# Performance work log

Measured on AMD Instinct MI355X. Metric: run time of the kernel, lower is better.

Reference implementation:

```python
import jax, jax.numpy as jnp
import numpy as np

N, E, G = 50000, 800000, 64
D, DE, DIN, L = 64, 4, 11, 2


def _lin(x, w, b):
    return x @ w + b


def _bn(x, g, b, eps=1e-5):
    # BatchNorm1d in training mode: biased batch statistics over dim 0
    m = x.mean(0)
    v = x.var(0)
    return (x - m) * jax.lax.rsqrt(v + eps) * g + b


def setup_inputs() -> dict:
    key = jax.random.key(0)
    ks = iter(jax.random.split(key, 64))

    def rn(shape, s=0.05):
        return jax.random.normal(next(ks), shape, jnp.float32) * s

    inp = dict(
        x=rn((N, DIN), 1.0),
        pos=rn((N, 3), 1.0),
        edge_attr=rn((E, DE), 1.0),
        edge_index=jax.random.randint(next(ks), (2, E), 0, N),
        batch=jnp.sort(jax.random.randint(next(ks), (N,), 0, G)),
        lin_in_w=rn((DIN, D)), lin_in_b=jnp.zeros((D,), jnp.float32),
        lin_pred_w=rn((D, 1)), lin_pred_b=jnp.zeros((1,), jnp.float32),
        # per-layer stacked params (leading dim L)
        msg_w1=rn((L, 2 * D + DE + 1, D)), msg_b1=jnp.zeros((L, D), jnp.float32),
        msg_g1=jnp.ones((L, D), jnp.float32), msg_be1=jnp.zeros((L, D), jnp.float32),
        msg_w2=rn((L, D, D)), msg_b2=jnp.zeros((L, D), jnp.float32),
        msg_g2=jnp.ones((L, D), jnp.float32), msg_be2=jnp.zeros((L, D), jnp.float32),
        pos_w1=rn((L, D, D)), pos_b1=jnp.zeros((L, D), jnp.float32),
        pos_g=jnp.ones((L, D), jnp.float32), pos_be=jnp.zeros((L, D), jnp.float32),
        pos_w2=rn((L, D, 1)), pos_b2=jnp.zeros((L, 1), jnp.float32),
        upd_w1=rn((L, 2 * D, D)), upd_b1=jnp.zeros((L, D), jnp.float32),
        upd_g1=jnp.ones((L, D), jnp.float32), upd_be1=jnp.zeros((L, D), jnp.float32),
        upd_w2=rn((L, D, D)), upd_b2=jnp.zeros((L, D), jnp.float32),
        upd_g2=jnp.ones((L, D), jnp.float32), upd_be2=jnp.zeros((L, D), jnp.float32),
    )
    return inp


def reference(x, pos, edge_attr, edge_index, batch,
              lin_in_w, lin_in_b, lin_pred_w, lin_pred_b,
              msg_w1, msg_b1, msg_g1, msg_be1, msg_w2, msg_b2, msg_g2, msg_be2,
              pos_w1, pos_b1, pos_g, pos_be, pos_w2, pos_b2,
              upd_w1, upd_b1, upd_g1, upd_be1, upd_w2, upd_b2, upd_g2, upd_be2):
    src, dst = edge_index[0], edge_index[1]  # h_j = h[src], h_i = h[dst]
    h = x @ lin_in_w + lin_in_b
    p = pos
    deg = jnp.maximum(jax.ops.segment_sum(jnp.ones((E,), h.dtype), dst, N), 1.0)
    for l in range(L):
        h_i, h_j = h[dst], h[src]          # (E, D) gathers
        pd = p[dst] - p[src]               # (E, 3)
        radial = jnp.sum(pd * pd, axis=1, keepdims=True)  # (E, 1)
        m = jnp.concatenate([h_i, h_j, radial, edge_attr], -1)  # (E, 2D+DE+1)
        m = jax.nn.relu(_bn(_lin(m, msg_w1[l], msg_b1[l]), msg_g1[l], msg_be1[l]))
        m = jax.nn.relu(_bn(_lin(m, msg_w2[l], msg_b2[l]), msg_g2[l], msg_be2[l]))
        s = jax.nn.relu(_bn(_lin(m, pos_w1[l], pos_b1[l]), pos_g[l], pos_be[l]))
        s = _lin(s, pos_w2[l], pos_b2[l])  # (E, 1) scalar gate
        pos_upd = pd * s                   # (E, 3)
        m_aggr = jax.ops.segment_sum(m, dst, N)                    # sum aggr
        p_aggr = jax.ops.segment_sum(pos_upd, dst, N) / deg[:, None]  # mean aggr
        u = jnp.concatenate([h, m_aggr], -1)
        u = jax.nn.relu(_bn(_lin(u, upd_w1[l], upd_b1[l]), upd_g1[l], upd_be1[l]))
        u = jax.nn.relu(_bn(_lin(u, upd_w2[l], upd_b2[l]), upd_g2[l], upd_be2[l]))
        h = h + u          # residual on node features (MPNNModel style)
        p = p + p_aggr     # position update from layer
    cnt = jnp.maximum(jax.ops.segment_sum(jnp.ones((N,), h.dtype), batch, G), 1.0)
    h_graph = jax.ops.segment_sum(h, batch, G) / cnt[:, None]  # global_mean_pool
    out = h_graph @ lin_pred_w + lin_pred_b
    return out.reshape(-1)
```

## Files before the change

### kernel.cpp

```cpp
#include <hip/hip_runtime.h>

#define Nn 50000
#define Ee 800000
#define Gg 64
#define Dd 64
#define KIN 133
#define ES 68
#define EPS 1e-5f

typedef unsigned short u16;

__device__ __forceinline__ u16 f2bf(float f) {
    union { float f; unsigned u; } v; v.f = f;
    unsigned r = (v.u + 0x7FFFu + ((v.u >> 16) & 1u)) >> 16;
    return (u16)r;
}
__device__ __forceinline__ float bf2f(u16 s) {
    union { unsigned u; float f; } v; v.u = ((unsigned)s) << 16;
    return v.f;
}


__global__ __launch_bounds__(256) void k_lin_in(const float* __restrict__ x,
    const float* __restrict__ W, const float* __restrict__ B, float* __restrict__ h)
{
    __shared__ float Ws[11 * 64];
    __shared__ float Bs[64];
    int t = threadIdx.x;
    for (int i = t; i < 11 * 64; i += 256) Ws[i] = W[i];
    if (t < 64) Bs[t] = B[t];
    __syncthreads();
    int i = blockIdx.x * 256 + t;
    if (i < Nn * 64) {
        int n = i >> 6, c = i & 63;
        float acc = Bs[c];
        #pragma unroll
        for (int k = 0; k < 11; k++) acc += x[n * 11 + k] * Ws[k * 64 + c];
        h[i] = acc;
    }
}

__global__ __launch_bounds__(256) void k_deg(const int* __restrict__ ei, float* __restrict__ deg)
{
    int e = blockIdx.x * 256 + threadIdx.x;
    if (e < Ee) atomicAdd(&deg[ei[Ee + e]], 1.f);
}

__global__ __launch_bounds__(256) void k_cnt(const int* __restrict__ batch, float* __restrict__ cnt)
{
    int n = blockIdx.x * 256 + threadIdx.x;
    if (n < Nn) atomicAdd(&cnt[batch[n]], 1.f);
}


__global__ __launch_bounds__(256) void k_edge_lin1(
    const float* __restrict__ h, const float* __restrict__ p,
    const float* __restrict__ ea, const int* __restrict__ ei,
    const float* __restrict__ W, const float* __restrict__ B,
    u16* __restrict__ ybuf, float* __restrict__ stats_out)
{
    __shared__ float Ws[KIN * 64];
    __shared__ float Bs[64];
    __shared__ float in_t[KIN * ES];
    int t = threadIdx.x;
    for (int i = t; i < KIN * 64; i += 256) Ws[i] = W[i];
    if (t < 64) Bs[t] = B[t];
    int tx = t & 15, ty = t >> 4;
    int c = t & 63, eg = t >> 6;
    float ssum[4] = {0, 0, 0, 0}, ssq[4] = {0, 0, 0, 0};
    for (int tile = blockIdx.x; tile < Ee / 64; tile += gridDim.x) {
        int te = tile * 64;
        __syncthreads();
        for (int e = eg; e < 64; e += 4) {
            int sr = ei[te + e], ds = ei[Ee + te + e];
            in_t[c * ES + e]        = h[(size_t)ds * 64 + c];
            in_t[(64 + c) * ES + e] = h[(size_t)sr * 64 + c];
        }
        if (t < 64) {
            int e = t;
            int sr = ei[te + e], ds = ei[Ee + te + e];
            float dx = p[ds * 3 + 0] - p[sr * 3 + 0];
            float dy = p[ds * 3 + 1] - p[sr * 3 + 1];
            float dz = p[ds * 3 + 2] - p[sr * 3 + 2];
            in_t[128 * ES + e] = dx * dx + dy * dy + dz * dz;
            float4 a4 = *(const float4*)&ea[(size_t)(te + e) * 4];
            in_t[129 * ES + e] = a4.x;
            in_t[130 * ES + e] = a4.y;
            in_t[131 * ES + e] = a4.z;
            in_t[132 * ES + e] = a4.w;
        }
        __syncthreads();
        float acc[4][4];
        #pragma unroll
        for (int i = 0; i < 4; i++)
            #pragma unroll
            for (int j = 0; j < 4; j++) acc[i][j] = Bs[4 * ty + j];
        for (int k = 0; k < KIN; k++) {
            float av[4], wv[4];
            *(float4*)av = *(const float4*)&in_t[k * ES + 4 * tx];
            *(float4*)wv = *(const float4*)&Ws[k * 64 + 4 * ty];
            #pragma unroll
            for (int i = 0; i < 4; i++)
                #pragma unroll
                for (int j = 0; j < 4; j++)
                    acc[i][j] += av[i] * wv[j];
        }
        #pragma unroll
        for (int i = 0; i < 4; i++) {
            size_t e = (size_t)te + 4 * tx + i;
            ushort4 o;
            o.x = f2bf(acc[i][0]); o.y = f2bf(acc[i][1]);
            o.z = f2bf(acc[i][2]); o.w = f2bf(acc[i][3]);
            *(ushort4*)&ybuf[e * 64 + 4 * ty] = o;
            float r0 = bf2f(o.x), r1 = bf2f(o.y), r2 = bf2f(o.z), r3 = bf2f(o.w);
            ssum[0] += r0; ssum[1] += r1; ssum[2] += r2; ssum[3] += r3;
            ssq[0] += r0 * r0; ssq[1] += r1 * r1; ssq[2] += r2 * r2; ssq[3] += r3 * r3;
        }
    }
    #pragma unroll
    for (int j = 0; j < 4; j++) {
        float s = ssum[j], q = ssq[j];
        #pragma unroll
        for (int o2 = 1; o2 < 16; o2 <<= 1) { s += __shfl_xor(s, o2); q += __shfl_xor(q, o2); }
        if (tx == 0) {
            atomicAdd(&stats_out[4 * ty + j], s);
            atomicAdd(&stats_out[64 + 4 * ty + j], q);
        }
    }
}


template<int AGGR>
__global__ __launch_bounds__(256) void k_edge_lin64(
    const float* __restrict__ stats_in, const float* __restrict__ gg,
    const float* __restrict__ be,
    const float* __restrict__ W, const float* __restrict__ B,
    const int* __restrict__ ei, float* __restrict__ magg,
    u16* __restrict__ ybuf, float* __restrict__ stats_out)
{
    __shared__ float Ws[64 * 64];
    __shared__ float As[64], Cs[64], Bs[64];
    __shared__ float in_t[64 * ES];
    int t = threadIdx.x;
    if (t < 64) {
        float mean = stats_in[t] * (1.f / Ee);
        float var  = stats_in[64 + t] * (1.f / Ee) - mean * mean;
        float a = gg[t] * rsqrtf(var + EPS);
        As[t] = a; Cs[t] = be[t] - mean * a; Bs[t] = B[t];
    }
    for (int i = t; i < 64 * 64; i += 256) Ws[i] = W[i];
    int tx = t & 15, ty = t >> 4;
    int c = t & 63, eg = t >> 6;
    float ssum[4] = {0, 0, 0, 0}, ssq[4] = {0, 0, 0, 0};
    for (int tile = blockIdx.x; tile < Ee / 64; tile += gridDim.x) {
        int te = tile * 64;
        __syncthreads();
        for (int e = eg; e < 64; e += 4) {
            float y = bf2f(ybuf[(size_t)(te + e) * 64 + c]);
            in_t[c * ES + e] = fmaxf(As[c] * y + Cs[c], 0.f);
        }
        __syncthreads();
        float acc[4][4];
        #pragma unroll
        for (int i = 0; i < 4; i++)
            #pragma unroll
            for (int j = 0; j < 4; j++) acc[i][j] = Bs[4 * ty + j];
        for (int k = 0; k < 64; k++) {
            float av[4], wv[4];
            *(float4*)av = *(const float4*)&in_t[k * ES + 4 * tx];
            *(float4*)wv = *(const float4*)&Ws[k * 64 + 4 * ty];
            #pragma unroll
            for (int i = 0; i < 4; i++)
                #pragma unroll
                for (int j = 0; j < 4; j++)
                    acc[i][j] += av[i] * wv[j];
        }
        if (AGGR) {
            for (int e = eg; e < 64; e += 4) {
                int ds = ei[Ee + te + e];
                atomicAdd(&magg[(size_t)ds * 64 + c], in_t[c * ES + e]);
            }
        }
        #pragma unroll
        for (int i = 0; i < 4; i++) {
            size_t e = (size_t)te + 4 * tx + i;
            ushort4 o;
            o.x = f2bf(acc[i][0]); o.y = f2bf(acc[i][1]);
            o.z = f2bf(acc[i][2]); o.w = f2bf(acc[i][3]);
            *(ushort4*)&ybuf[e * 64 + 4 * ty] = o;
            float r0 = bf2f(o.x), r1 = bf2f(o.y), r2 = bf2f(o.z), r3 = bf2f(o.w);
            ssum[0] += r0; ssum[1] += r1; ssum[2] += r2; ssum[3] += r3;
            ssq[0] += r0 * r0; ssq[1] += r1 * r1; ssq[2] += r2 * r2; ssq[3] += r3 * r3;
        }
    }
    #pragma unroll
    for (int j = 0; j < 4; j++) {
        float s = ssum[j], q = ssq[j];
        #pragma unroll
        for (int o2 = 1; o2 < 16; o2 <<= 1) { s += __shfl_xor(s, o2); q += __shfl_xor(q, o2); }
        if (tx == 0) {
            atomicAdd(&stats_out[4 * ty + j], s);
            atomicAdd(&stats_out[64 + 4 * ty + j], q);
        }
    }
}


__global__ __launch_bounds__(256) void k_pos2(
    const float* __restrict__ stats_in, const float* __restrict__ gg, const float* __restrict__ be,
    const float* __restrict__ W2, const float* __restrict__ B2,
    const float* __restrict__ p, const int* __restrict__ ei,
    const u16* __restrict__ ybuf, float* __restrict__ pagg)
{
    __shared__ float As[64], Cs[64], Ws[64];
    int t = threadIdx.x;
    if (t < 64) {
        float mean = stats_in[t] * (1.f / Ee);
        float var  = stats_in[64 + t] * (1.f / Ee) - mean * mean;
        float a = gg[t] * rsqrtf(var + EPS);
        As[t] = a; Cs[t] = be[t] - mean * a; Ws[t] = W2[t];
    }
    __syncthreads();
    int e = blockIdx.x * 256 + t;
    if (e >= Ee) return;
    float acc = B2[0];
    const u16* row = &ybuf[(size_t)e * 64];
    #pragma unroll
    for (int u = 0; u < 16; u++) {
        ushort4 y4 = *(const ushort4*)&row[4 * u];
        acc += fmaxf(As[4 * u + 0] * bf2f(y4.x) + Cs[4 * u + 0], 0.f) * Ws[4 * u + 0]
             + fmaxf(As[4 * u + 1] * bf2f(y4.y) + Cs[4 * u + 1], 0.f) * Ws[4 * u + 1]
             + fmaxf(As[4 * u + 2] * bf2f(y4.z) + Cs[4 * u + 2], 0.f) * Ws[4 * u + 2]
             + fmaxf(As[4 * u + 3] * bf2f(y4.w) + Cs[4 * u + 3], 0.f) * Ws[4 * u + 3];
    }
    int sr = ei[e], ds = ei[Ee + e];
    float dx = p[ds * 3 + 0] - p[sr * 3 + 0];
    float dy = p[ds * 3 + 1] - p[sr * 3 + 1];
    float dz = p[ds * 3 + 2] - p[sr * 3 + 2];
    atomicAdd(&pagg[ds * 3 + 0], dx * acc);
    atomicAdd(&pagg[ds * 3 + 1], dy * acc);
    atomicAdd(&pagg[ds * 3 + 2], dz * acc);
}


__global__ __launch_bounds__(256) void k_node_lin1(
    const float* __restrict__ h, const float* __restrict__ magg,
    const float* __restrict__ W, const float* __restrict__ B,
    float* __restrict__ yn, float* __restrict__ stats_out)
{
    __shared__ float Ws[128 * 64];
    __shared__ float Bs[64];
    __shared__ float in_t[128 * ES];
    int t = threadIdx.x;
    for (int i = t; i < 128 * 64; i += 256) Ws[i] = W[i];
    if (t < 64) Bs[t] = B[t];
    int tx = t & 15, ty = t >> 4, c = t & 63, eg = t >> 6;
    float ssum[4] = {0, 0, 0, 0}, ssq[4] = {0, 0, 0, 0};
    int nT = (Nn + 63) / 64;
    for (int tile = blockIdx.x; tile < nT; tile += gridDim.x) {
        int te = tile * 64;
        __syncthreads();
        for (int e = eg; e < 64; e += 4) {
            int n = te + e;
            bool v = n < Nn;
            in_t[c * ES + e]        = v ? h[(size_t)n * 64 + c]    : 0.f;
            in_t[(64 + c) * ES + e] = v ? magg[(size_t)n * 64 + c] : 0.f;
        }
        __syncthreads();
        float acc[4][4];
        #pragma unroll
        for (int i = 0; i < 4; i++)
            #pragma unroll
            for (int j = 0; j < 4; j++) acc[i][j] = Bs[4 * ty + j];
        for (int k = 0; k < 128; k++) {
            float av[4], wv[4];
            *(float4*)av = *(const float4*)&in_t[k * ES + 4 * tx];
            *(float4*)wv = *(const float4*)&Ws[k * 64 + 4 * ty];
            #pragma unroll
            for (int i = 0; i < 4; i++)
                #pragma unroll
                for (int j = 0; j < 4; j++)
                    acc[i][j] += av[i] * wv[j];
        }
        #pragma unroll
        for (int i = 0; i < 4; i++) {
            int n = te + 4 * tx + i;
            if (n < Nn) {
                float4 o; o.x = acc[i][0]; o.y = acc[i][1]; o.z = acc[i][2]; o.w = acc[i][3];
                *(float4*)&yn[(size_t)n * 64 + 4 * ty] = o;
                #pragma unroll
                for (int j = 0; j < 4; j++) { ssum[j] += acc[i][j]; ssq[j] += acc[i][j] * acc[i][j]; }
            }
        }
    }
    #pragma unroll
    for (int j = 0; j < 4; j++) {
        float s = ssum[j], q = ssq[j];
        #pragma unroll
        for (int o2 = 1; o2 < 16; o2 <<= 1) { s += __shfl_xor(s, o2); q += __shfl_xor(q, o2); }
        if (tx == 0) {
            atomicAdd(&stats_out[4 * ty + j], s);
            atomicAdd(&stats_out[64 + 4 * ty + j], q);
        }
    }
}


__global__ __launch_bounds__(256) void k_node_lin64(
    const float* __restrict__ stats_in, const float* __restrict__ gg, const float* __restrict__ be,
    const float* __restrict__ W, const float* __restrict__ B,
    float* __restrict__ yn, float* __restrict__ stats_out)
{
    __shared__ float Ws[64 * 64];
    __shared__ float As[64], Cs[64], Bs[64];
    __shared__ float in_t[64 * ES];
    int t = threadIdx.x;
    if (t < 64) {
        float mean = stats_in[t] * (1.f / Nn);
        float var  = stats_in[64 + t] * (1.f / Nn) - mean * mean;
        float a = gg[t] * rsqrtf(var + EPS);
        As[t] = a; Cs[t] = be[t] - mean * a; Bs[t] = B[t];
    }
    for (int i = t; i < 64 * 64; i += 256) Ws[i] = W[i];
    int tx = t & 15, ty = t >> 4, c = t & 63, eg = t >> 6;
    float ssum[4] = {0, 0, 0, 0}, ssq[4] = {0, 0, 0, 0};
    int nT = (Nn + 63) / 64;
    for (int tile = blockIdx.x; tile < nT; tile += gridDim.x) {
        int te = tile * 64;
        __syncthreads();
        for (int e = eg; e < 64; e += 4) {
            int n = te + e;
            float y = (n < Nn) ? yn[(size_t)n * 64 + c] : 0.f;
            in_t[c * ES + e] = fmaxf(As[c] * y + Cs[c], 0.f);
        }
        __syncthreads();
        float acc[4][4];
        #pragma unroll
        for (int i = 0; i < 4; i++)
            #pragma unroll
            for (int j = 0; j < 4; j++) acc[i][j] = Bs[4 * ty + j];
        for (int k = 0; k < 64; k++) {
            float av[4], wv[4];
            *(float4*)av = *(const float4*)&in_t[k * ES + 4 * tx];
            *(float4*)wv = *(const float4*)&Ws[k * 64 + 4 * ty];
            #pragma unroll
            for (int i = 0; i < 4; i++)
                #pragma unroll
                for (int j = 0; j < 4; j++)
                    acc[i][j] += av[i] * wv[j];
        }
        #pragma unroll
        for (int i = 0; i < 4; i++) {
            int n = te + 4 * tx + i;
            if (n < Nn) {
                float4 o; o.x = acc[i][0]; o.y = acc[i][1]; o.z = acc[i][2]; o.w = acc[i][3];
                *(float4*)&yn[(size_t)n * 64 + 4 * ty] = o;
                #pragma unroll
                for (int j = 0; j < 4; j++) { ssum[j] += acc[i][j]; ssq[j] += acc[i][j] * acc[i][j]; }
            }
        }
    }
    #pragma unroll
    for (int j = 0; j < 4; j++) {
        float s = ssum[j], q = ssq[j];
        #pragma unroll
        for (int o2 = 1; o2 < 16; o2 <<= 1) { s += __shfl_xor(s, o2); q += __shfl_xor(q, o2); }
        if (tx == 0) {
            atomicAdd(&stats_out[4 * ty + j], s);
            atomicAdd(&stats_out[64 + 4 * ty + j], q);
        }
    }
}


__global__ __launch_bounds__(256) void k_node_update(
    const float* __restrict__ stats_in, const float* __restrict__ gg, const float* __restrict__ be,
    const float* __restrict__ yn, float* __restrict__ h,
    const float* __restrict__ p_in, float* __restrict__ p_out,
    const float* __restrict__ pagg, const float* __restrict__ deg)
{
    int i = blockIdx.x * 256 + threadIdx.x;
    if (i < Nn * 64) {
        int c = i & 63;
        float mean = stats_in[c] * (1.f / Nn);
        float var  = stats_in[64 + c] * (1.f / Nn) - mean * mean;
        float a = gg[c] * rsqrtf(var + EPS);
        float cc = be[c] - mean * a;
        h[i] += fmaxf(a * yn[i] + cc, 0.f);
    }
    if (i < Nn * 3) {
        float dg = fmaxf(deg[i / 3], 1.f);
        p_out[i] = p_in[i] + pagg[i] / dg;
    }
}


__global__ __launch_bounds__(256) void k_pool(const int* __restrict__ batch,
    const float* __restrict__ h, float* __restrict__ pool)
{
    int i = blockIdx.x * 256 + threadIdx.x;
    if (i < Nn * 64) {
        int n = i >> 6, c = i & 63;
        atomicAdd(&pool[(size_t)batch[n] * 64 + c], h[i]);
    }
}

__global__ void k_out(const float* __restrict__ pool, const float* __restrict__ cnt,
    const float* __restrict__ W, const float* __restrict__ B, float* __restrict__ out)
{
    int g = threadIdx.x;
    if (g < 64) {
        float acc = 0.f;
        for (int c = 0; c < 64; c++) acc += pool[g * 64 + c] * W[c];
        out[g] = acc / fmaxf(cnt[g], 1.f) + B[0];
    }
}


extern "C" void kernel_launch(void* const* d_in, const int* in_sizes, int n_in,
                              void* d_out, int out_size, void* d_ws, size_t ws_size,
                              hipStream_t stream)
{
    const float* x        = (const float*)d_in[0];
    const float* pos      = (const float*)d_in[1];
    const float* ea       = (const float*)d_in[2];
    const int*   ei       = (const int*)  d_in[3];
    const int*   batch    = (const int*)  d_in[4];
    const float* lin_in_w = (const float*)d_in[5];
    const float* lin_in_b = (const float*)d_in[6];
    const float* lin_pr_w = (const float*)d_in[7];
    const float* lin_pr_b = (const float*)d_in[8];
    const float* msg_w1   = (const float*)d_in[9];
    const float* msg_b1   = (const float*)d_in[10];
    const float* msg_g1   = (const float*)d_in[11];
    const float* msg_be1  = (const float*)d_in[12];
    const float* msg_w2   = (const float*)d_in[13];
    const float* msg_b2   = (const float*)d_in[14];
    const float* msg_g2   = (const float*)d_in[15];
    const float* msg_be2  = (const float*)d_in[16];
    const float* pos_w1   = (const float*)d_in[17];
    const float* pos_b1   = (const float*)d_in[18];
    const float* pos_g    = (const float*)d_in[19];
    const float* pos_be   = (const float*)d_in[20];
    const float* pos_w2   = (const float*)d_in[21];
    const float* pos_b2   = (const float*)d_in[22];
    const float* upd_w1   = (const float*)d_in[23];
    const float* upd_b1   = (const float*)d_in[24];
    const float* upd_g1   = (const float*)d_in[25];
    const float* upd_be1  = (const float*)d_in[26];
    const float* upd_w2   = (const float*)d_in[27];
    const float* upd_b2   = (const float*)d_in[28];
    const float* upd_g2   = (const float*)d_in[29];
    const float* upd_be2  = (const float*)d_in[30];
    float* out = (float*)d_out;

    float* ws = (float*)d_ws;
    size_t o = 0;
    float* h    = ws + o; o += (size_t)Nn * 64;
    u16*   ybuf = (u16*)(ws + o); o += (size_t)Ee * 64;
    float* yn   = ws + o; o += (size_t)Nn * 64;
    float* magg = ws + o; o += (size_t)Nn * 64;
    float* pagg = ws + o; o += (size_t)Nn * 3;
    float* pws  = ws + o; o += (size_t)Nn * 3;
    float* stats= ws + o; o += 1280;
    float* pool = ws + o; o += 64 * 64;
    float* cnt  = ws + o; o += 64;
    float* deg  = ws + o; o += Nn;
    if (ws_size < o * sizeof(float)) return;

    hipMemsetAsync(stats, 0, (size_t)(1280 + 64 * 64 + 64 + Nn) * sizeof(float), stream);
    k_lin_in<<<(Nn * 64 + 255) / 256, 256, 0, stream>>>(x, lin_in_w, lin_in_b, h);
    k_deg<<<(Ee + 255) / 256, 256, 0, stream>>>(ei, deg);
    k_cnt<<<(Nn + 255) / 256, 256, 0, stream>>>(batch, cnt);

    for (int l = 0; l < 2; l++) {
        hipMemsetAsync(magg, 0, ((size_t)Nn * 64 + (size_t)Nn * 3) * sizeof(float), stream);
        const float* pc = (l == 0) ? pos : pws;
        float* st = stats + (size_t)l * 5 * 128;
        k_edge_lin1<<<512, 256, 0, stream>>>(h, pc, ea, ei,
            msg_w1 + (size_t)l * KIN * 64, msg_b1 + l * 64, ybuf, st + 0 * 128);
        k_edge_lin64<0><<<1024, 256, 0, stream>>>(st + 0 * 128, msg_g1 + l * 64, msg_be1 + l * 64,
            msg_w2 + (size_t)l * 64 * 64, msg_b2 + l * 64, ei, nullptr, ybuf, st + 1 * 128);
        k_edge_lin64<1><<<1024, 256, 0, stream>>>(st + 1 * 128, msg_g2 + l * 64, msg_be2 + l * 64,
            pos_w1 + (size_t)l * 64 * 64, pos_b1 + l * 64, ei, magg, ybuf, st + 2 * 128);
        k_pos2<<<(Ee + 255) / 256, 256, 0, stream>>>(st + 2 * 128, pos_g + l * 64, pos_be + l * 64,
            pos_w2 + l * 64, pos_b2 + l, pc, ei, ybuf, pagg);
        k_node_lin1<<<782, 256, 0, stream>>>(h, magg,
            upd_w1 + (size_t)l * 128 * 64, upd_b1 + l * 64, yn, st + 3 * 128);
        k_node_lin64<<<782, 256, 0, stream>>>(st + 3 * 128, upd_g1 + l * 64, upd_be1 + l * 64,
            upd_w2 + (size_t)l * 64 * 64, upd_b2 + l * 64, yn, st + 4 * 128);
        k_node_update<<<(Nn * 64 + 255) / 256, 256, 0, stream>>>(st + 4 * 128,
            upd_g2 + l * 64, upd_be2 + l * 64, yn, h, pc, pws, pagg, deg);
    }
    k_pool<<<(Nn * 64 + 255) / 256, 256, 0, stream>>>(batch, h, pool);
    k_out<<<1, 64, 0, stream>>>(pool, cnt, lin_pr_w, lin_pr_b, out);
}
```

Baseline: 2.476 ms.

## Use bf16 MFMA for edge 64x64 linear layers with bf16 LDS tiles

```diff
diff --git a/kernel.cpp b/kernel.cpp
--- a/kernel.cpp
+++ b/kernel.cpp
@@ -2,13 +2,13 @@
 
 #define Nn 50000
 #define Ee 800000
-#define Gg 64
-#define Dd 64
 #define KIN 133
 #define ES 68
 #define EPS 1e-5f
 
 typedef unsigned short u16;
+typedef __attribute__((ext_vector_type(8))) short bf16x8;
+typedef __attribute__((ext_vector_type(4))) float f32x4;
 
 __device__ __forceinline__ u16 f2bf(float f) {
     union { float f; unsigned u; } v; v.f = f;
@@ -138,69 +138,97 @@
     const int* __restrict__ ei, float* __restrict__ magg,
     u16* __restrict__ ybuf, float* __restrict__ stats_out)
 {
-    __shared__ float Ws[64 * 64];
+    __shared__ u16 At[64 * 72];
+    __shared__ u16 Wt[64 * 72];
     __shared__ float As[64], Cs[64], Bs[64];
-    __shared__ float in_t[64 * ES];
     int t = threadIdx.x;
+    int lane = t & 63, w = t >> 6;
+    int col16 = lane & 15, kg = lane >> 4;
+
     if (t < 64) {
         float mean = stats_in[t] * (1.f / Ee);
         float var  = stats_in[64 + t] * (1.f / Ee) - mean * mean;
         float a = gg[t] * rsqrtf(var + EPS);
         As[t] = a; Cs[t] = be[t] - mean * a; Bs[t] = B[t];
     }
-    for (int i = t; i < 64 * 64; i += 256) Ws[i] = W[i];
-    int tx = t & 15, ty = t >> 4;
-    int c = t & 63, eg = t >> 6;
+    {
+        int col = t & 63, k0 = (t >> 6) * 16;
+        for (int k = k0; k < k0 + 16; k++)
+            Wt[col * 72 + k] = f2bf(W[k * 64 + col]);
+    }
+    __syncthreads();
+
+    bf16x8 bfA[4], bfB[4];
+    #pragma unroll
+    for (int cb = 0; cb < 4; cb++) {
+        const u16* wp = &Wt[(16 * cb + col16) * 72 + 8 * kg];
+        bfA[cb] = *(const bf16x8*)&wp[0];
+        bfB[cb] = *(const bf16x8*)&wp[32];
+    }
+
+    int eRow = t >> 2;
+    int gq = t & 3;
     float ssum[4] = {0, 0, 0, 0}, ssq[4] = {0, 0, 0, 0};
+
     for (int tile = blockIdx.x; tile < Ee / 64; tile += gridDim.x) {
         int te = tile * 64;
-        __syncthreads();
-        for (int e = eg; e < 64; e += 4) {
-            float y = bf2f(ybuf[(size_t)(te + e) * 64 + c]);
-            in_t[c * ES + e] = fmaxf(As[c] * y + Cs[c], 0.f);
-        }
-        __syncthreads();
-        float acc[4][4];
-        #pragma unroll
-        for (int i = 0; i < 4; i++)
-            #pragma unroll
-            for (int j = 0; j < 4; j++) acc[i][j] = Bs[4 * ty + j];
-        for (int k = 0; k < 64; k++) {
-            float av[4], wv[4];
-            *(float4*)av = *(const float4*)&in_t[k * ES + 4 * tx];
-            *(float4*)wv = *(const float4*)&Ws[k * 64 + 4 * ty];
-            #pragma unroll
-            for (int i = 0; i < 4; i++)
-                #pragma unroll
-                for (int j = 0; j < 4; j++)
-                    acc[i][j] += av[i] * wv[j];
+        const u16* src = &ybuf[(size_t)(te + eRow) * 64 + 16 * gq];
+        bf16x8 y0 = *(const bf16x8*)&src[0];
+        bf16x8 y1 = *(const bf16x8*)&src[8];
+        __syncthreads();
+        bf16x8 m0, m1;
+        #pragma unroll
+        for (int j = 0; j < 8; j++) {
+            int c0 = 16 * gq + j, c1 = c0 + 8;
+            float v0 = fmaxf(As[c0] * bf2f((u16)y0[j]) + Cs[c0], 0.f);
+            float v1 = fmaxf(As[c1] * bf2f((u16)y1[j]) + Cs[c1], 0.f);
+            m0[j] = (short)f2bf(v0);
+            m1[j] = (short)f2bf(v1);
+        }
+        *(bf16x8*)&At[eRow * 72 + 16 * gq] = m0;
+        *(bf16x8*)&At[eRow * 72 + 16 * gq + 8] = m1;
+        __syncthreads();
+
+        const u16* ap = &At[(16 * w + col16) * 72 + 8 * kg];
+        bf16x8 a0 = *(const bf16x8*)&ap[0];
+        bf16x8 a1 = *(const bf16x8*)&ap[32];
+        #pragma unroll
+        for (int cb = 0; cb < 4; cb++) {
+            f32x4 acc;
+            float bv = Bs[16 * cb + col16];
+            acc[0] = bv; acc[1] = bv; acc[2] = bv; acc[3] = bv;
+            acc = __builtin_amdgcn_mfma_f32_16x16x32_bf16(a0, bfA[cb], acc, 0, 0, 0);
+            acc = __builtin_amdgcn_mfma_f32_16x16x32_bf16(a1, bfB[cb], acc, 0, 0, 0);
+            #pragma unroll
+            for (int r = 0; r < 4; r++) {
+                u16 ob = f2bf(acc[r]);
+                int erow = te + 16 * w + 4 * kg + r;
+                ybuf[(size_t)erow * 64 + 16 * cb + col16] = ob;
+                float rv = bf2f(ob);
+                ssum[cb] += rv; ssq[cb] += rv * rv;
+            }
         }
         if (AGGR) {
-            for (int e = eg; e < 64; e += 4) {
-                int ds = ei[Ee + te + e];
-                atomicAdd(&magg[(size_t)ds * 64 + c], in_t[c * ES + e]);
+            int dnode = ei[Ee + te + lane];
+            const u16* mp = &At[lane * 72 + 16 * w];
+            bf16x8 v0 = *(const bf16x8*)&mp[0];
+            bf16x8 v1 = *(const bf16x8*)&mp[8];
+            float* mg = &magg[(size_t)dnode * 64 + 16 * w];
+            #pragma unroll
+            for (int j = 0; j < 8; j++) {
+                atomicAdd(&mg[j],     bf2f((u16)v0[j]));
+                atomicAdd(&mg[8 + j], bf2f((u16)v1[j]));
             }
         }
-        #pragma unroll
-        for (int i = 0; i < 4; i++) {
-            size_t e = (size_t)te + 4 * tx + i;
-            ushort4 o;
-            o.x = f2bf(acc[i][0]); o.y = f2bf(acc[i][1]);
-            o.z = f2bf(acc[i][2]); o.w = f2bf(acc[i][3]);
-            *(ushort4*)&ybuf[e * 64 + 4 * ty] = o;
-            float r0 = bf2f(o.x), r1 = bf2f(o.y), r2 = bf2f(o.z), r3 = bf2f(o.w);
-            ssum[0] += r0; ssum[1] += r1; ssum[2] += r2; ssum[3] += r3;
-            ssq[0] += r0 * r0; ssq[1] += r1 * r1; ssq[2] += r2 * r2; ssq[3] += r3 * r3;
-        }
     }
     #pragma unroll
-    for (int j = 0; j < 4; j++) {
-        float s = ssum[j], q = ssq[j];
-        #pragma unroll
-        for (int o2 = 1; o2 < 16; o2 <<= 1) { s += __shfl_xor(s, o2); q += __shfl_xor(q, o2); }
-        if (tx == 0) {
-            atomicAdd(&stats_out[4 * ty + j], s);
-            atomicAdd(&stats_out[64 + 4 * ty + j], q);
+    for (int cb = 0; cb < 4; cb++) {
+        float s = ssum[cb], q = ssq[cb];
+        s += __shfl_xor(s, 16); q += __shfl_xor(q, 16);
+        s += __shfl_xor(s, 32); q += __shfl_xor(q, 32);
+        if (kg == 0) {
+            atomicAdd(&stats_out[16 * cb + col16], s);
+            atomicAdd(&stats_out[64 + 16 * cb + col16], q);
         }
     }
 }
@@ -479,9 +507,9 @@
         float* st = stats + (size_t)l * 5 * 128;
         k_edge_lin1<<<512, 256, 0, stream>>>(h, pc, ea, ei,
             msg_w1 + (size_t)l * KIN * 64, msg_b1 + l * 64, ybuf, st + 0 * 128);
-        k_edge_lin64<0><<<1024, 256, 0, stream>>>(st + 0 * 128, msg_g1 + l * 64, msg_be1 + l * 64,
+        k_edge_lin64<0><<<2048, 256, 0, stream>>>(st + 0 * 128, msg_g1 + l * 64, msg_be1 + l * 64,
             msg_w2 + (size_t)l * 64 * 64, msg_b2 + l * 64, ei, nullptr, ybuf, st + 1 * 128);
-        k_edge_lin64<1><<<1024, 256, 0, stream>>>(st + 1 * 128, msg_g2 + l * 64, msg_be2 + l * 64,
+        k_edge_lin64<1><<<2048, 256, 0, stream>>>(st + 1 * 128, msg_g2 + l * 64, msg_be2 + l * 64,
             pos_w1 + (size_t)l * 64 * 64, pos_b1 + l * 64, ei, magg, ybuf, st + 2 * 128);
         k_pos2<<<(Ee + 255) / 256, 256, 0, stream>>>(st + 2 * 128, pos_g + l * 64, pos_be + l * 64,
             pos_w2 + l * 64, pos_b2 + l, pc, ei, ybuf, pagg);
```

After: 7.448 ms. 3.01x slower.
